# Kernel optimization log

Hardware: AMD Instinct MI355X
Metric: run time of the kernel (lower is better)

Reference implementation:

```python
import jax, jax.numpy as jnp
import numpy as np

N = 200000   # nodes
E = 6400000  # edges
F = 128      # input features
H = 16       # hidden dim (fixed in module)
C = 10       # num classes
B = 512      # graphs in batch


def setup_inputs() -> dict:
    key = jax.random.key(0)
    ks = jax.random.split(key, 9)
    x = jax.random.normal(ks[0], (N, F), dtype=jnp.float32)
    edge_index = jax.random.randint(ks[1], (2, E), 0, N, dtype=jnp.int64)
    batch = jnp.sort(jax.random.randint(ks[2], (N,), 0, B, dtype=jnp.int64))
    W1 = jax.random.normal(ks[3], (F, H), dtype=jnp.float32) * 0.1
    b1 = jnp.zeros((H,), dtype=jnp.float32)
    W2 = jax.random.normal(ks[4], (H, H), dtype=jnp.float32) * 0.1
    b2 = jnp.zeros((H,), dtype=jnp.float32)
    Wfc = jax.random.normal(ks[5], (H, C), dtype=jnp.float32) * 0.1
    bfc = jnp.zeros((C,), dtype=jnp.float32)
    return {"x": x, "edge_index": edge_index, "batch": batch,
            "W1": W1, "b1": b1, "W2": W2, "b2": b2, "Wfc": Wfc, "bfc": bfc}


def reference(x, edge_index, batch, W1, b1, W2, b2, Wfc, bfc):
    row, col = edge_index[0], edge_index[1]  # source -> target
    ones_e = jnp.ones((E,), dtype=x.dtype)
    # GCN symmetric norm with implicit self-loops: deg = 1 + in-degree
    deg = 1.0 + jax.ops.segment_sum(ones_e, col, num_segments=N)
    dis = deg ** -0.5                         # [N]
    norm = dis[row] * dis[col]                # [E], self-loop norm = 1/deg

    def gcn_conv(h, W, b):
        hw = h @ W                             # [N, out]
        msg = norm[:, None] * hw[row]          # [E, out]
        agg = jax.ops.segment_sum(msg, col, num_segments=N)
        agg = agg + hw * (1.0 / deg)[:, None]  # self-loop contribution
        return agg + b

    h = jax.nn.relu(gcn_conv(x, W1, b1))
    h = gcn_conv(h, W2, b2)
    # global mean pool over graphs
    ones_n = jnp.ones((N,), dtype=h.dtype)
    counts = jax.ops.segment_sum(ones_n, batch, num_segments=B)
    sums = jax.ops.segment_sum(h, batch, num_segments=B)
    pooled = sums / jnp.maximum(counts, 1.0)[:, None]  # [B, H]
    return pooled @ Wfc + bfc                           # [B, C]
```

## Files before the change

### kernel.cpp

```cpp
#include <hip/hip_runtime.h>

#define N_ 200000
#define E_ 6400000
#define F_ 128
#define H_ 16
#define C_ 10
#define B_ 512

#define CSH   15
#define NCH   7
#define SBSH  10
#define NSB   196
#define NKEY  (NCH * NSB)
#define NT    256
#define EPT   25000
#define N1    (N_ + 1)
#define STG2  6144
#define AGGB  1563
#define G1B   1563
#define QSTR  516

__global__ __launch_bounds__(1024) void k_count1(const int* __restrict__ row, const int* __restrict__ col,
                                                 int* __restrict__ cnt1) {
    __shared__ int hist[NKEY];
    int tid = threadIdx.x, tile = blockIdx.x;
    for (int i = tid; i < NKEY; i += 1024) hist[i] = 0;
    __syncthreads();
    const int* r = row + (size_t)tile * EPT;
    const int* c = col + (size_t)tile * EPT;
    for (int i = tid; i < EPT; i += 1024) {
        int key = (r[i] >> CSH) * NSB + (c[i] >> SBSH);
        atomicAdd(&hist[key], 1);
    }
    __syncthreads();
    for (int i = tid; i < NKEY; i += 1024) cnt1[(size_t)i * NT + tile] = hist[i];
}

__global__ __launch_bounds__(256) void k_scan_col(int* __restrict__ cnt_mat, int* __restrict__ keyTotal) {
    __shared__ int s[256];
    int k = blockIdx.x, t = threadIdx.x;
    int v[4];
    int seg = 0;
#pragma unroll
    for (int j = 0; j < 4; ++j) {
        int idx = 4 * t + j;
        v[j] = (idx < NT) ? cnt_mat[(size_t)k * NT + idx] : 0;
        seg += v[j];
    }
    s[t] = seg;
    __syncthreads();
    for (int off = 1; off < 256; off <<= 1) {
        int tmp = (t >= off) ? s[t - off] : 0;
        __syncthreads();
        s[t] += tmp;
        __syncthreads();
    }
    if (t == 255) keyTotal[k] = s[255];
    int running = s[t] - seg;
#pragma unroll
    for (int j = 0; j < 4; ++j) {
        int idx = 4 * t + j;
        if (idx < NT) {
            int old = v[j];
            cnt_mat[(size_t)k * NT + idx] = running;
            running += old;
        }
    }
}

__global__ __launch_bounds__(1024) void k_scan_top(const int* __restrict__ keyTotal, int* __restrict__ keyStart, int n) {
    __shared__ int s[1024];
    __shared__ int base;
    int t = threadIdx.x;
    if (t == 0) base = 0;
    __syncthreads();
    int ntile = (n + 1023) / 1024;
    for (int tile = 0; tile < ntile; ++tile) {
        int idx = tile * 1024 + t;
        int v = (idx < n) ? keyTotal[idx] : 0;
        s[t] = v;
        __syncthreads();
        for (int off = 1; off < 1024; off <<= 1) {
            int tmp = (t >= off) ? s[t - off] : 0;
            __syncthreads();
            s[t] += tmp;
            __syncthreads();
        }
        if (idx < n) keyStart[idx] = base + s[t] - v;
        __syncthreads();
        if (t == 0) base += s[1023];
        __syncthreads();
    }
    if (t == 0) keyStart[n] = base;
}

__global__ __launch_bounds__(1024) void k_part1(const int* __restrict__ row, const int* __restrict__ col,
                                                const int* __restrict__ cnt1, const int* __restrict__ ks1,
                                                unsigned int* __restrict__ esrc) {
    __shared__ int cur[NKEY];
    int tid = threadIdx.x, tile = blockIdx.x;
    for (int i = tid; i < NKEY; i += 1024) cur[i] = cnt1[(size_t)i * NT + tile] + ks1[i];
    __syncthreads();
    const int* r = row + (size_t)tile * EPT;
    const int* c = col + (size_t)tile * EPT;
    for (int i = tid; i < EPT; i += 1024) {
        int src = r[i], dst = c[i];
        int key = (src >> CSH) * NSB + (dst >> SBSH);
        int p = atomicAdd(&cur[key], 1);
        esrc[p] = ((unsigned int)(dst & 1023) << CSH) | (unsigned int)(src & 32767);
    }
}

__global__ __launch_bounds__(512) void k_part2(const unsigned int* __restrict__ esrc, const int* __restrict__ ks1,
                                               unsigned short* __restrict__ off16, unsigned int* __restrict__ edges) {
    __shared__ unsigned int stg[STG2];
    __shared__ int cnt[1024];
    __shared__ int aux[512];
    int b = blockIdx.x, tid = threadIdx.x;
    int c = b / NSB, sb = b % NSB;
    int s = ks1[b], e = ks1[b + 1], len = e - s;
    if (sb == NSB - 1 && tid == 0) off16[(size_t)c * N1 + N_] = (unsigned short)len;
    cnt[tid] = 0;
    cnt[tid + 512] = 0;
    __syncthreads();
    for (int i = tid; i < len; i += 512) atomicAdd(&cnt[esrc[s + i] >> CSH], 1);
    __syncthreads();
    int base = tid * 2;
    int v0 = cnt[base], v1 = cnt[base + 1];
    int run = v0 + v1;
    aux[tid] = run;
    __syncthreads();
    for (int o = 1; o < 512; o <<= 1) {
        int tmp = (tid >= o) ? aux[tid - o] : 0;
        __syncthreads();
        aux[tid] += tmp;
        __syncthreads();
    }
    int acc = aux[tid] - run;
    int nb = (sb << SBSH) + base;
    cnt[base] = acc;
    if (nb < N_) off16[(size_t)c * N1 + nb] = (unsigned short)acc;
    acc += v0;
    cnt[base + 1] = acc;
    if (nb + 1 < N_) off16[(size_t)c * N1 + nb + 1] = (unsigned short)acc;
    __syncthreads();
    if (len <= STG2) {
        for (int i = tid; i < len; i += 512) {
            unsigned int w = esrc[s + i];
            int pos = atomicAdd(&cnt[w >> CSH], 1);
            stg[pos] = ((unsigned int)c << CSH) | (w & 32767u);
        }
        __syncthreads();
        for (int i = tid; i < len; i += 512) edges[s + i] = stg[i];
    } else {
        for (int i = tid; i < len; i += 512) {
            unsigned int w = esrc[s + i];
            int pos = atomicAdd(&cnt[w >> CSH], 1);
            edges[s + pos] = ((unsigned int)c << CSH) | (w & 32767u);
        }
    }
}

__global__ __launch_bounds__(256) void k_gemm1s(const float* __restrict__ x, const float* __restrict__ W1,
                                                const unsigned short* __restrict__ off16, const int* __restrict__ ks1g,
                                                float* __restrict__ dis, float* __restrict__ P) {
    __shared__ float wsh[4 * QSTR];
    __shared__ int ks[NKEY + 1];
    for (int i = threadIdx.x; i < F_ * H_; i += 256) {
        int r = i >> 4, h = i & 15;
        int qq = (r >> 2) & 3, jj = r >> 4, mm = r & 3;
        wsh[qq * QSTR + (jj * 4 + mm) * 16 + h] = W1[i];
    }
    for (int i = threadIdx.x; i <= NKEY; i += 256) ks[i] = ks1g[i];
    __syncthreads();
    int t = blockIdx.x * 256 + threadIdx.x;
    int p = t >> 2, q = t & 3;
    int n0 = p * 2;
    if (n0 >= N_) return;
    int sb00 = n0 >> SBSH, sb01 = (n0 + 1) >> SBSH, sbE = (n0 + 2) >> SBSH;
    int deg0 = 0, deg1 = 0;
    for (int c = q; c < NCH; c += 4) {
        const unsigned short* ob = off16 + (size_t)c * N1 + n0;
        ushort2 o2 = *(const ushort2*)ob;
        unsigned short oE = ob[2];
        deg0 += (ks[c * NSB + sb01] + o2.y) - (ks[c * NSB + sb00] + o2.x);
        deg1 += (ks[c * NSB + sbE] + oE) - (ks[c * NSB + sb01] + o2.y);
    }
    deg0 += __shfl_xor(deg0, 1); deg0 += __shfl_xor(deg0, 2);
    deg1 += __shfl_xor(deg1, 1); deg1 += __shfl_xor(deg1, 2);
    float dn0 = rsqrtf(1.0f + (float)deg0);
    float dn1 = rsqrtf(1.0f + (float)deg1);
    if (q == 0) dis[n0] = dn0;
    if (q == 1) dis[n0 + 1] = dn1;
    const float4* xr0 = (const float4*)(x + (size_t)n0 * F_);
    const float4* xr1 = (const float4*)(x + (size_t)(n0 + 1) * F_);
    const float4* wq = (const float4*)(wsh + q * QSTR);
    float4 a0q0 = {0,0,0,0}, a0q1 = {0,0,0,0}, a0q2 = {0,0,0,0}, a0q3 = {0,0,0,0};
    float4 a1q0 = {0,0,0,0}, a1q1 = {0,0,0,0}, a1q2 = {0,0,0,0}, a1q3 = {0,0,0,0};
#define KSTEP(RL, XS0, XS1)                                                        \
    {                                                                              \
        float4 w0 = wq[(RL) * 4 + 0], w1 = wq[(RL) * 4 + 1];                       \
        float4 w2 = wq[(RL) * 4 + 2], w3 = wq[(RL) * 4 + 3];                       \
        a0q0.x += (XS0) * w0.x; a0q0.y += (XS0) * w0.y; a0q0.z += (XS0) * w0.z; a0q0.w += (XS0) * w0.w; \
        a0q1.x += (XS0) * w1.x; a0q1.y += (XS0) * w1.y; a0q1.z += (XS0) * w1.z; a0q1.w += (XS0) * w1.w; \
        a0q2.x += (XS0) * w2.x; a0q2.y += (XS0) * w2.y; a0q2.z += (XS0) * w2.z; a0q2.w += (XS0) * w2.w; \
        a0q3.x += (XS0) * w3.x; a0q3.y += (XS0) * w3.y; a0q3.z += (XS0) * w3.z; a0q3.w += (XS0) * w3.w; \
        a1q0.x += (XS1) * w0.x; a1q0.y += (XS1) * w0.y; a1q0.z += (XS1) * w0.z; a1q0.w += (XS1) * w0.w; \
        a1q1.x += (XS1) * w1.x; a1q1.y += (XS1) * w1.y; a1q1.z += (XS1) * w1.z; a1q1.w += (XS1) * w1.w; \
        a1q2.x += (XS1) * w2.x; a1q2.y += (XS1) * w2.y; a1q2.z += (XS1) * w2.z; a1q2.w += (XS1) * w2.w; \
        a1q3.x += (XS1) * w3.x; a1q3.y += (XS1) * w3.y; a1q3.z += (XS1) * w3.z; a1q3.w += (XS1) * w3.w; \
    }
#pragma unroll
    for (int j = 0; j < 8; ++j) {
        float4 xa = xr0[j * 4 + q];
        float4 xb = xr1[j * 4 + q];
        int rb = j * 4;
        KSTEP(rb + 0, xa.x, xb.x)
        KSTEP(rb + 1, xa.y, xb.y)
        KSTEP(rb + 2, xa.z, xb.z)
        KSTEP(rb + 3, xa.w, xb.w)
    }
#undef KSTEP
#define RED(F)                                                                     \
    F.x += __shfl_xor(F.x, 1); F.y += __shfl_xor(F.y, 1); F.z += __shfl_xor(F.z, 1); F.w += __shfl_xor(F.w, 1); \
    F.x += __shfl_xor(F.x, 2); F.y += __shfl_xor(F.y, 2); F.z += __shfl_xor(F.z, 2); F.w += __shfl_xor(F.w, 2);
    RED(a0q0) RED(a0q1) RED(a0q2) RED(a0q3)
    RED(a1q0) RED(a1q1) RED(a1q2) RED(a1q3)
#undef RED
    float4 s0 = (q == 0) ? a0q0 : (q == 1) ? a0q1 : (q == 2) ? a0q2 : a0q3;
    float4 s1 = (q == 0) ? a1q0 : (q == 1) ? a1q1 : (q == 2) ? a1q2 : a1q3;
    float4* P4 = (float4*)P;
    float4 o0, o1;
    o0.x = s0.x * dn0; o0.y = s0.y * dn0; o0.z = s0.z * dn0; o0.w = s0.w * dn0;
    o1.x = s1.x * dn1; o1.y = s1.y * dn1; o1.z = s1.z * dn1; o1.w = s1.w * dn1;
    P4[(size_t)n0 * 4 + q] = o0;
    P4[(size_t)(n0 + 1) * 4 + q] = o1;
}

__global__ __launch_bounds__(256) void k_gemm2s(const float* __restrict__ hin, const float* __restrict__ W2,
                                                const float* __restrict__ dis, float* __restrict__ P) {
    __shared__ float w[H_ * H_];
    if (threadIdx.x < H_ * H_) w[threadIdx.x] = W2[threadIdx.x];
    __syncthreads();
    int n = blockIdx.x * 256 + threadIdx.x;
    if (n >= N_) return;
    float hv[H_];
    const float4* hr = reinterpret_cast<const float4*>(hin + (size_t)n * H_);
#pragma unroll
    for (int q = 0; q < 4; ++q) {
        float4 v = hr[q];
        hv[q * 4 + 0] = v.x; hv[q * 4 + 1] = v.y; hv[q * 4 + 2] = v.z; hv[q * 4 + 3] = v.w;
    }
    float acc[H_];
#pragma unroll
    for (int h = 0; h < H_; ++h) acc[h] = 0.f;
#pragma unroll
    for (int k = 0; k < H_; ++k)
#pragma unroll
        for (int h = 0; h < H_; ++h) acc[h] += hv[k] * w[k * H_ + h];
    float dn = dis[n];
    float* o = P + (size_t)n * H_;
#pragma unroll
    for (int h = 0; h < H_; h += 4)
        *(float4*)(o + h) = make_float4(acc[h] * dn, acc[h + 1] * dn, acc[h + 2] * dn, acc[h + 3] * dn);
}

template <int RELU>
__global__ __launch_bounds__(256) void k_agg(const float4* __restrict__ P4, const unsigned int* __restrict__ csr,
                                             const unsigned short* __restrict__ off16, const int* __restrict__ ks1g,
                                             const float* __restrict__ dis, const float* __restrict__ bias,
                                             float4* __restrict__ Q4) {
    __shared__ int ks[NKEY + 1];
    for (int i = threadIdx.x; i <= NKEY; i += 256) ks[i] = ks1g[i];
    __syncthreads();
    int g = threadIdx.x >> 2, hq = threadIdx.x & 3;
    int n0 = blockIdx.x * 128 + g * 2;
    if (n0 >= N_) return;
    int sb  = n0 >> SBSH;
    int sbE = (n0 + 2) >> SBSH;
    float4 acc0 = {0,0,0,0}, acc1 = {0,0,0,0};
    const unsigned short* ob = off16 + n0;
    ushort2 o2 = *(const ushort2*)ob;
    unsigned short oE = ob[2];
#pragma unroll
    for (int c = 0; c < NCH; ++c) {
        int bs = ks[c * NSB + sb];
        int be = ks[c * NSB + sbE];
        int s0 = bs + o2.x;
        int s1 = bs + o2.y;
        int e1 = be + oE;
        if (c + 1 < NCH) {
            const unsigned short* obn = off16 + (size_t)(c + 1) * N1 + n0;
            o2 = *(const ushort2*)obn;
            oE = obn[2];
        }
#pragma unroll 4
        for (int p = s0; p < e1; ++p) {
            float4 v = P4[(size_t)csr[p] * 4 + hq];
            float w0 = (p < s1) ? 1.f : 0.f;
            float w1 = 1.f - w0;
            acc0.x += w0 * v.x; acc0.y += w0 * v.y; acc0.z += w0 * v.z; acc0.w += w0 * v.w;
            acc1.x += w1 * v.x; acc1.y += w1 * v.y; acc1.z += w1 * v.z; acc1.w += w1 * v.w;
        }
    }
    float2 d2 = *(const float2*)(dis + n0);
    float4 b4 = ((const float4*)bias)[hq];
#define FINISH(ACC, K, DN)                                            \
    {                                                                 \
        float4 self = P4[(size_t)(n0 + K) * 4 + hq];                  \
        float4 v;                                                     \
        v.x = (DN) * (ACC.x + self.x) + b4.x;                         \
        v.y = (DN) * (ACC.y + self.y) + b4.y;                         \
        v.z = (DN) * (ACC.z + self.z) + b4.z;                         \
        v.w = (DN) * (ACC.w + self.w) + b4.w;                         \
        if (RELU) {                                                   \
            v.x = fmaxf(v.x, 0.f); v.y = fmaxf(v.y, 0.f);             \
            v.z = fmaxf(v.z, 0.f); v.w = fmaxf(v.w, 0.f);             \
        }                                                             \
        Q4[(size_t)(n0 + K) * 4 + hq] = v;                            \
    }
    FINISH(acc0, 0, d2.x)
    FINISH(acc1, 1, d2.y)
#undef FINISH
}

__global__ __launch_bounds__(256) void k_pool_fc(const float* __restrict__ h2, const int* __restrict__ batch,
                                                 const float* __restrict__ Wfc, const float* __restrict__ bfc,
                                                 float* __restrict__ out) {
    int b = blockIdx.x;
    int lo = 0, hi = N_;
    while (lo < hi) { int m = (lo + hi) >> 1; if (batch[m] < b) lo = m + 1; else hi = m; }
    int start = lo;
    lo = start; hi = N_;
    while (lo < hi) { int m = (lo + hi) >> 1; if (batch[m] < b + 1) lo = m + 1; else hi = m; }
    int end = lo;

    int t = threadIdx.x;
    int h = t & 15, q = t >> 4;
    float acc = 0.f;
    for (int n = start + q; n < end; n += 16) acc += h2[(size_t)n * H_ + h];
    acc += __shfl_xor(acc, 16);
    acc += __shfl_xor(acc, 32);

    __shared__ float part[4][H_];
    __shared__ float pooled[H_];
    if ((t & 63) < 16) part[t >> 6][h] = acc;
    __syncthreads();
    if (t < H_) {
        float s2 = part[0][t] + part[1][t] + part[2][t] + part[3][t];
        pooled[t] = s2 / fmaxf((float)(end - start), 1.0f);
    }
    __syncthreads();
    if (t < C_) {
        float o = bfc[t];
#pragma unroll
        for (int hh = 0; hh < H_; ++hh) o += pooled[hh] * Wfc[hh * C_ + t];
        out[b * C_ + t] = o;
    }
}

extern "C" void kernel_launch(void* const* d_in, const int* in_sizes, int n_in,
                              void* d_out, int out_size, void* d_ws, size_t ws_size,
                              hipStream_t stream) {
    const float* x    = (const float*)d_in[0];
    const int*   ei   = (const int*)d_in[1];
    const int*   batch= (const int*)d_in[2];
    const float* W1   = (const float*)d_in[3];
    const float* b1   = (const float*)d_in[4];
    const float* W2   = (const float*)d_in[5];
    const float* b2   = (const float*)d_in[6];
    const float* Wfc  = (const float*)d_in[7];
    const float* bfc  = (const float*)d_in[8];
    float* out = (float*)d_out;

    const int* row = ei;
    const int* col = ei + E_;

    size_t off = 0;
    auto alloc = [&](size_t bytes) -> void* {
        void* p = (char*)d_ws + off;
        off += (bytes + 255) & ~(size_t)255;
        return p;
    };
    char*           U        = (char*)alloc((size_t)NCH * N1 * 2);
    int*            cnt1     = (int*)U;
    unsigned short* off16    = (unsigned short*)U;
    int*            keyTotal = (int*)alloc((size_t)NKEY * 4);
    int*            ks1      = (int*)alloc((size_t)(NKEY + 1) * 4);
    unsigned int*   edges    = (unsigned int*)alloc((size_t)E_ * 4);
    float*          dis      = (float*)alloc((size_t)N_ * 4);
    float*          P        = (float*)alloc((size_t)N_ * H_ * 4);
    float*          Q        = (float*)alloc((size_t)N_ * H_ * 4);
    unsigned int*   esrc     = (unsigned int*)P;
    (void)ws_size; (void)in_sizes; (void)n_in; (void)out_size;

    const int gridN = (N_ + 255) / 256;

    k_count1  <<<NT, 1024, 0, stream>>>(row, col, cnt1);
    k_scan_col<<<NKEY, 256, 0, stream>>>(cnt1, keyTotal);
    k_scan_top<<<1, 1024, 0, stream>>>(keyTotal, ks1, NKEY);
    k_part1   <<<NT, 1024, 0, stream>>>(row, col, cnt1, ks1, esrc);
    k_part2   <<<NKEY, 512, 0, stream>>>(esrc, ks1, off16, edges);

    k_gemm1s<<<G1B, 256, 0, stream>>>(x, W1, off16, ks1, dis, P);
    k_agg<1><<<AGGB, 256, 0, stream>>>((const float4*)P, edges, off16, ks1, dis, b1, (float4*)Q);
    k_gemm2s<<<gridN, 256, 0, stream>>>(Q, W2, dis, P);
    k_agg<0><<<AGGB, 256, 0, stream>>>((const float4*)P, edges, off16, ks1, dis, b2, (float4*)Q);

    k_pool_fc<<<B_, 256, 0, stream>>>(Q, batch, Wfc, bfc, out);
}
```

Before: 268.9 us.

## Coarsen first-pass partition to 2048-node superblocks, split into halves in second pass

The first radix partition pass now buckets edges by 2048-destination superblocks, which halves the key count and so the shared histogram, the count matrix and the scan work. The second pass launches two blocks per superblock. Each block filters its half, builds local offsets and writes a per-block start array (ks10) that downstream kernels use. The cost is that each second-pass block reads twice as many edges and discards half of them.

```diff
diff --git a/kernel.cpp b/kernel.cpp
--- a/kernel.cpp
+++ b/kernel.cpp
@@ -12,6 +12,8 @@
 #define SBSH  10
 #define NSB   196
 #define NKEY  (NCH * NSB)
+#define NSB11 98
+#define NKEY11 (NCH * NSB11)
 #define NT    256
 #define EPT   25000
 #define N1    (N_ + 1)
@@ -22,18 +24,18 @@
 
 __global__ __launch_bounds__(1024) void k_count1(const int* __restrict__ row, const int* __restrict__ col,
                                                  int* __restrict__ cnt1) {
-    __shared__ int hist[NKEY];
+    __shared__ int hist[NKEY11];
     int tid = threadIdx.x, tile = blockIdx.x;
-    for (int i = tid; i < NKEY; i += 1024) hist[i] = 0;
+    for (int i = tid; i < NKEY11; i += 1024) hist[i] = 0;
     __syncthreads();
     const int* r = row + (size_t)tile * EPT;
     const int* c = col + (size_t)tile * EPT;
     for (int i = tid; i < EPT; i += 1024) {
-        int key = (r[i] >> CSH) * NSB + (c[i] >> SBSH);
+        int key = (r[i] >> CSH) * NSB11 + (c[i] >> 11);
         atomicAdd(&hist[key], 1);
     }
     __syncthreads();
-    for (int i = tid; i < NKEY; i += 1024) cnt1[(size_t)i * NT + tile] = hist[i];
+    for (int i = tid; i < NKEY11; i += 1024) cnt1[(size_t)i * NT + tile] = hist[i];
 }
 
 __global__ __launch_bounds__(256) void k_scan_col(int* __restrict__ cnt_mat, int* __restrict__ keyTotal) {
@@ -95,35 +97,39 @@
 }
 
 __global__ __launch_bounds__(1024) void k_part1(const int* __restrict__ row, const int* __restrict__ col,
-                                                const int* __restrict__ cnt1, const int* __restrict__ ks1,
+                                                const int* __restrict__ cnt1, const int* __restrict__ ks686,
                                                 unsigned int* __restrict__ esrc) {
-    __shared__ int cur[NKEY];
+    __shared__ int cur[NKEY11];
     int tid = threadIdx.x, tile = blockIdx.x;
-    for (int i = tid; i < NKEY; i += 1024) cur[i] = cnt1[(size_t)i * NT + tile] + ks1[i];
+    for (int i = tid; i < NKEY11; i += 1024) cur[i] = cnt1[(size_t)i * NT + tile] + ks686[i];
     __syncthreads();
     const int* r = row + (size_t)tile * EPT;
     const int* c = col + (size_t)tile * EPT;
     for (int i = tid; i < EPT; i += 1024) {
         int src = r[i], dst = c[i];
-        int key = (src >> CSH) * NSB + (dst >> SBSH);
+        int key = (src >> CSH) * NSB11 + (dst >> 11);
         int p = atomicAdd(&cur[key], 1);
-        esrc[p] = ((unsigned int)(dst & 1023) << CSH) | (unsigned int)(src & 32767);
-    }
-}
-
-__global__ __launch_bounds__(512) void k_part2(const unsigned int* __restrict__ esrc, const int* __restrict__ ks1,
-                                               unsigned short* __restrict__ off16, unsigned int* __restrict__ edges) {
+        esrc[p] = ((unsigned int)(dst & 2047) << CSH) | (unsigned int)(src & 32767);
+    }
+}
+
+__global__ __launch_bounds__(512) void k_part2(const unsigned int* __restrict__ esrc, const int* __restrict__ ks686,
+                                               int* __restrict__ ks10, unsigned short* __restrict__ off16,
+                                               unsigned int* __restrict__ edges) {
     __shared__ unsigned int stg[STG2];
     __shared__ int cnt[1024];
     __shared__ int aux[512];
     int b = blockIdx.x, tid = threadIdx.x;
-    int c = b / NSB, sb = b % NSB;
-    int s = ks1[b], e = ks1[b + 1], len = e - s;
-    if (sb == NSB - 1 && tid == 0) off16[(size_t)c * N1 + N_] = (unsigned short)len;
+    int c = b / NSB, rem = b % NSB;
+    int sb11 = rem >> 1, h = rem & 1;
+    int s = ks686[c * NSB11 + sb11], e = ks686[c * NSB11 + sb11 + 1], len = e - s;
     cnt[tid] = 0;
     cnt[tid + 512] = 0;
     __syncthreads();
-    for (int i = tid; i < len; i += 512) atomicAdd(&cnt[esrc[s + i] >> CSH], 1);
+    for (int i = tid; i < len; i += 512) {
+        unsigned int dl = esrc[s + i] >> CSH;
+        if ((int)(dl >> 10) == h) atomicAdd(&cnt[dl & 1023], 1);
+    }
     __syncthreads();
     int base = tid * 2;
     int v0 = cnt[base], v1 = cnt[base + 1];
@@ -136,27 +142,40 @@
         aux[tid] += tmp;
         __syncthreads();
     }
+    int total = aux[511];
     int acc = aux[tid] - run;
-    int nb = (sb << SBSH) + base;
+    int nb = (rem << SBSH) + base;
     cnt[base] = acc;
     if (nb < N_) off16[(size_t)c * N1 + nb] = (unsigned short)acc;
     acc += v0;
     cnt[base + 1] = acc;
     if (nb + 1 < N_) off16[(size_t)c * N1 + nb + 1] = (unsigned short)acc;
     __syncthreads();
-    if (len <= STG2) {
+    int myStart = s + h * (len - total);
+    if (tid == 0) {
+        ks10[b] = myStart;
+        if (b == NKEY - 1) ks10[NKEY] = myStart + total;
+        if (rem == NSB - 1) off16[(size_t)c * N1 + N_] = (unsigned short)total;
+    }
+    if (total <= STG2) {
         for (int i = tid; i < len; i += 512) {
             unsigned int w = esrc[s + i];
-            int pos = atomicAdd(&cnt[w >> CSH], 1);
-            stg[pos] = ((unsigned int)c << CSH) | (w & 32767u);
-        }
-        __syncthreads();
-        for (int i = tid; i < len; i += 512) edges[s + i] = stg[i];
+            unsigned int dl = w >> CSH;
+            if ((int)(dl >> 10) == h) {
+                int pos = atomicAdd(&cnt[dl & 1023], 1);
+                stg[pos] = ((unsigned int)c << CSH) | (w & 32767u);
+            }
+        }
+        __syncthreads();
+        for (int i = tid; i < total; i += 512) edges[myStart + i] = stg[i];
     } else {
         for (int i = tid; i < len; i += 512) {
             unsigned int w = esrc[s + i];
-            int pos = atomicAdd(&cnt[w >> CSH], 1);
-            edges[s + pos] = ((unsigned int)c << CSH) | (w & 32767u);
+            unsigned int dl = w >> CSH;
+            if ((int)(dl >> 10) == h) {
+                int pos = atomicAdd(&cnt[dl & 1023], 1);
+                edges[myStart + pos] = ((unsigned int)c << CSH) | (w & 32767u);
+            }
         }
     }
 }
@@ -385,8 +404,9 @@
     char*           U        = (char*)alloc((size_t)NCH * N1 * 2);
     int*            cnt1     = (int*)U;
     unsigned short* off16    = (unsigned short*)U;
-    int*            keyTotal = (int*)alloc((size_t)NKEY * 4);
-    int*            ks1      = (int*)alloc((size_t)(NKEY + 1) * 4);
+    int*            keyTotal = (int*)alloc((size_t)NKEY11 * 4);
+    int*            ks686    = (int*)alloc((size_t)(NKEY11 + 1) * 4);
+    int*            ks10     = (int*)alloc((size_t)(NKEY + 1) * 4);
     unsigned int*   edges    = (unsigned int*)alloc((size_t)E_ * 4);
     float*          dis      = (float*)alloc((size_t)N_ * 4);
     float*          P        = (float*)alloc((size_t)N_ * H_ * 4);
@@ -397,15 +417,15 @@
     const int gridN = (N_ + 255) / 256;
 
     k_count1  <<<NT, 1024, 0, stream>>>(row, col, cnt1);
-    k_scan_col<<<NKEY, 256, 0, stream>>>(cnt1, keyTotal);
-    k_scan_top<<<1, 1024, 0, stream>>>(keyTotal, ks1, NKEY);
-    k_part1   <<<NT, 1024, 0, stream>>>(row, col, cnt1, ks1, esrc);
-    k_part2   <<<NKEY, 512, 0, stream>>>(esrc, ks1, off16, edges);
-
-    k_gemm1s<<<G1B, 256, 0, stream>>>(x, W1, off16, ks1, dis, P);
-    k_agg<1><<<AGGB, 256, 0, stream>>>((const float4*)P, edges, off16, ks1, dis, b1, (float4*)Q);
+    k_scan_col<<<NKEY11, 256, 0, stream>>>(cnt1, keyTotal);
+    k_scan_top<<<1, 1024, 0, stream>>>(keyTotal, ks686, NKEY11);
+    k_part1   <<<NT, 1024, 0, stream>>>(row, col, cnt1, ks686, esrc);
+    k_part2   <<<NKEY, 512, 0, stream>>>(esrc, ks686, ks10, off16, edges);
+
+    k_gemm1s<<<G1B, 256, 0, stream>>>(x, W1, off16, ks10, dis, P);
+    k_agg<1><<<AGGB, 256, 0, stream>>>((const float4*)P, edges, off16, ks10, dis, b1, (float4*)Q);
     k_gemm2s<<<gridN, 256, 0, stream>>>(Q, W2, dis, P);
-    k_agg<0><<<AGGB, 256, 0, stream>>>((const float4*)P, edges, off16, ks1, dis, b2, (float4*)Q);
+    k_agg<0><<<AGGB, 256, 0, stream>>>((const float4*)P, edges, off16, ks10, dis, b2, (float4*)Q);
 
     k_pool_fc<<<B_, 256, 0, stream>>>(Q, batch, Wfc, bfc, out);
 }
```

New measurement: 265.0 us (median of 2 runs). Within noise of the previous version (-1.4%).
